# Kernel optimization log

Measured on AMD Instinct MI355X. Metric: run time of the kernel, lower is better.

## Reference

```python
import jax, jax.numpy as jnp
import numpy as np

C_IN, C_OUT, H = 8, 8, 16
N1D = 20                      # 1D quadrature points -> 400 mesh nodes in 2D
B = 16
DECAY = (N1D / 4.0) ** 4      # set_quad: decay_param = (N/4)**4


def _quad_mesh():
    # Gauss-Legendre nodes/weights on [-1,1], tensor-product in 2D (get_quad_mesh)
    x, w = np.polynomial.legendre.leggauss(N1D)
    X, Y = np.meshgrid(x, x, indexing='xy')
    WX, WY = np.meshgrid(w, w, indexing='xy')
    nodes = np.dstack([X, Y]).reshape(-1, 2).astype(np.float32)
    weights = (WX * WY).reshape(-1).astype(np.float32)
    return nodes, weights


def setup_inputs() -> dict:
    key = jax.random.key(0)
    k1, k2, k3, k4 = jax.random.split(key, 4)
    nodes, w = _quad_mesh()
    K = C_IN * C_OUT
    return {
        'features': jax.random.normal(k1, (B, C_IN, N1D * N1D), jnp.float32),
        # 64 tiny MLPs (Linear no bias + Sin), spec (2,16,16,1), stacked on axis 0
        'W1': jax.random.normal(k2, (K, H, 2), jnp.float32) / np.sqrt(2.0),
        'W2': jax.random.normal(k3, (K, H, H), jnp.float32) / np.sqrt(float(H)),
        'W3': jax.random.normal(k4, (K, 1, H), jnp.float32) / np.sqrt(float(H)),
        'output_locs': jnp.asarray(nodes),   # (M,2) same tensor-product mesh
        'mesh_nodes': jnp.asarray(nodes),    # (N,2)
        'mesh_weights': jnp.asarray(w),      # (N,) product of 1D weights
    }


def _kernel(W1, W2, W3, output_locs, mesh_nodes):
    # pairwise eval points z = y_m - x_n, shape (M, N, 2)
    z = output_locs[:, None, :] - mesh_nodes[None, :, :]
    M, N, _ = z.shape
    zf = z.reshape(M * N, 2)
    # batched tiny MLPs: Linear -> Sin -> Linear -> Sin -> Linear (no bias)
    h = jnp.sin(jnp.einsum('khd,pd->kph', W1, zf))
    h = jnp.sin(jnp.einsum('koh,kph->kpo', W2, h))
    kv = jnp.einsum('koh,kph->kpo', W3, h)[..., 0]          # (K, M*N)
    # bump function enforcing compact support: exp(1 - 1/(1 - c*||z||^4))
    bump_arg = jnp.sum(zf * zf, axis=-1) ** 2               # ||z||^4
    inside = bump_arg < 1.0 / DECAY
    safe = jnp.where(inside, 1.0 - DECAY * bump_arg, 1.0)
    bump = jnp.where(inside, jnp.exp(1.0 - 1.0 / safe), 0.0)
    kv = kv * bump[None, :]
    return kv.reshape(C_OUT, C_IN, M, N)


def reference(features, W1, W2, W3, output_locs, mesh_nodes, mesh_weights):
    Kmat = _kernel(W1, W2, W3, output_locs, mesh_nodes)     # (Co,Ci,M,N)
    # quadrature-weighted conv sum: out[b,o,m] = sum_{i,n} K[o,i,m,n] w[n] f[b,i,n]
    return jnp.einsum('oimn,n,bin->bom', Kmat, mesh_weights, features)
```

## Files before the change

### kernel.cpp

```cpp
#include <hip/hip_runtime.h>
#include <math.h>

#define CIN   8
#define COUT  8
#define HH    16
#define NN    400
#define MM    400
#define BB    16

#define THREADS 512
#define PMAX    32
#define NGRP    16
#define MPG     25
#define PPG     16
#define NPAGES  (NGRP*PPG)
#define MAXNM   12

#define WS_FT   0
#define WS_L    (NN*CIN*BB)
#define WS_CNT  (WS_L + MM*PMAX*4)
#define WS_PM0  (WS_CNT + MM)
#define WS_PNM  (WS_PM0 + NPAGES)

__device__ __forceinline__ bool bump_inside(float zx, float zy, float& a) {
    float s = __fadd_rn(__fmul_rn(zx, zx), __fmul_rn(zy, zy));
    a = __fmul_rn(s, s);
    return a < (1.0f / 625.0f);
}

__global__ __launch_bounds__(THREADS) void prep_kernel(
    const float* __restrict__ f,
    const float* __restrict__ locs,
    const float* __restrict__ nodes,
    const float* __restrict__ wq,
    float* __restrict__ ws)
{
    const int blk = blockIdx.x;
    const int t   = threadIdx.x;

    if (blk < 100) {
        int idx = blk * 512 + t;
        int b = idx / 3200;
        int r = idx - b * 3200;
        int i = r / 400;
        int n = r - i * 400;
        ws[WS_FT + n*128 + i*16 + b] = f[idx];
    } else if (blk < 150) {
        const int lane = t & 63;
        const int w    = t >> 6;
        const int m    = (blk - 100) * 8 + w;
        const float2 y = ((const float2*)locs)[m];
        const float2* nd = (const float2*)nodes;
        float4* lst = (float4*)(ws + WS_L);
        int cnt = 0;
        for (int n0 = 0; n0 < NN; n0 += 64) {
            int n = n0 + lane;
            bool in = false;
            float zx = 0.f, zy = 0.f, bwv = 0.f;
            if (n < NN) {
                float2 x = nd[n];
                zx = y.x - x.x; zy = y.y - x.y;
                float a;
                if (bump_inside(zx, zy, a)) {
                    in = true;
                    bwv = __expf(1.0f - 1.0f/(1.0f - 625.0f*a)) * wq[n];
                }
            }
            unsigned long long msk = __ballot(in);
            int idx = cnt + __popcll(msk & ((1ull << lane) - 1ull));
            if (in && idx < PMAX)
                lst[m*PMAX + idx] = make_float4(zx, zy, bwv, __int_as_float(n));
            cnt += __popcll(msk);
        }
        if (lane >= cnt && lane < PMAX)
            lst[m*PMAX + lane] = make_float4(0.f, 0.f, 0.f, __int_as_float(0));
    } else {
        __shared__ float dx2[400], dy2[400];
        __shared__ int   scnt[400];
        if (t < 400) {
            int i = t / 20, j = t % 20;
            float zx = locs[2*i]          - nodes[2*j];
            float zy = locs[2*(i*20) + 1] - nodes[2*(j*20) + 1];
            dx2[t] = __fmul_rn(zx, zx);
            dy2[t] = __fmul_rn(zy, zy);
        }
        __syncthreads();
        if (t < 400) {
            int mx = t % 20, my = t / 20;
            int c = 0;
            for (int ny = 0; ny < 20; ++ny) {
                float dyv = dy2[my*20 + ny];
                for (int nx = 0; nx < 20; ++nx) {
                    float s = __fadd_rn(dx2[mx*20 + nx], dyv);
                    float a = __fmul_rn(s, s);
                    c += (a < (1.0f / 625.0f)) ? 1 : 0;
                }
            }
            c = min(c, PMAX);
            scnt[t] = c;
            ((int*)ws)[WS_CNT + t] = c;
        }
        __syncthreads();
        if (t < NGRP) {
            int* pm0 = (int*)ws + WS_PM0;
            int* pnm = (int*)ws + WS_PNM;
            const int m0g = t * MPG, mend = m0g + MPG;
            int p = t * PPG;
            int cur0 = m0g, used = 0;
            for (int m = m0g; m < mend; ++m) {
                int c = scnt[m];
                if (used + c > 64) {
                    pm0[p] = cur0; pnm[p] = m - cur0; ++p;
                    cur0 = m; used = 0;
                }
                used += c;
            }
            pm0[p] = cur0; pnm[p] = mend - cur0; ++p;
            for (; p < (t + 1) * PPG; ++p) { pm0[p] = 0; pnm[p] = 0; }
        }
    }
}

__global__ __launch_bounds__(THREADS) void quadconv_kernel(
    const float* __restrict__ W1,
    const float* __restrict__ W2,
    const float* __restrict__ W3,
    const float* __restrict__ ws,
    float* __restrict__ out)
{
    __shared__ float s_w2[8*256];
    __shared__ float s_w1[8*32];
    __shared__ float s_w3[8*16];
    __shared__ float s_kv[8*64];
    __shared__ int   s_pn[64];
    __shared__ int   s_off[MAXNM + 1];
    __shared__ int   s_m0;

    const int t    = threadIdx.x;
    const int lane = t & 63;
    const int w    = __builtin_amdgcn_readfirstlane(t >> 6);
    const int p    = blockIdx.x >> 3;
    const int kg   = blockIdx.x & 7;

    const int nm = ((const int*)ws)[WS_PNM + p];
    if (nm == 0) return;

    {
        const float4* W2v = (const float4*)(W2 + kg * 8 * 256);
        ((float4*)s_w2)[t] = W2v[t];
        if (t < 64) ((float4*)s_w1)[t] = ((const float4*)(W1 + kg * 8 * 32))[t];
        if (t < 32) ((float4*)s_w3)[t] = ((const float4*)(W3 + kg * 8 * 16))[t];
    }
    if (t == 0) {
        int m0 = ((const int*)ws)[WS_PM0 + p];
        s_m0 = m0;
        int off = 0;
        s_off[0] = 0;
        for (int j = 0; j < nm; ++j) {
            off += ((const int*)ws)[WS_CNT + m0 + j];
            s_off[j + 1] = off;
        }
    }
    __syncthreads();

    int seg = 0;
    #pragma unroll
    for (int sgi = 1; sgi < MAXNM; ++sgi)
        seg += (sgi < nm && lane >= s_off[sgi]) ? 1 : 0;
    const int used = s_off[nm];
    float4 sv = make_float4(0.f, 0.f, 0.f, 0.f);
    int n_id = 0;
    if (lane < used) {
        const int m  = s_m0 + seg;
        const int jj = lane - s_off[seg];
        sv = ((const float4*)(ws + WS_L))[m * PMAX + jj];
        n_id = __float_as_int(sv.w);
    }
    if (t < 64) s_pn[t] = n_id;

    {
        const float* __restrict__ w1 = s_w1 + w * 32;
        const float* __restrict__ w2 = s_w2 + w * 256;
        const float* __restrict__ w3 = s_w3 + w * 16;
        const float zx = sv.x, zy = sv.y, bw = sv.z;

        float h1[HH];
        #pragma unroll
        for (int j = 0; j < HH; ++j)
            h1[j] = __sinf(w1[2*j] * zx + w1[2*j + 1] * zy);

        float kv = 0.f;
        #pragma unroll
        for (int oo = 0; oo < HH; ++oo) {
            float d = 0.f;
            #pragma unroll
            for (int j = 0; j < HH; ++j)
                d += w2[oo*HH + j] * h1[j];
            kv += w3[oo] * __sinf(d);
        }
        s_kv[w*64 + lane] = kv * bw;
    }
    __syncthreads();

    if (t < nm * 16) {
        const int b    = t & 15;
        const int sidx = t >> 4;
        const int lo   = s_off[sidx];
        const int L    = s_off[sidx + 1] - lo;
        const float* __restrict__ ftp = ws + WS_FT;
        float acc = 0.f;
        for (int j = 0; j < L; ++j) {
            const int n = s_pn[lo + j];
            const float* fb = ftp + n*128 + b;
            #pragma unroll
            for (int ww = 0; ww < 8; ++ww)
                acc += s_kv[ww*64 + lo + j] * fb[ww*16];
        }
        out[b * (COUT*MM) + kg * MM + (s_m0 + sidx)] = acc;
    }
}

extern "C" void kernel_launch(void* const* d_in, const int* in_sizes, int n_in,
                              void* d_out, int out_size, void* d_ws, size_t ws_size,
                              hipStream_t stream) {
    const float* f     = (const float*)d_in[0];
    const float* W1    = (const float*)d_in[1];
    const float* W2    = (const float*)d_in[2];
    const float* W3    = (const float*)d_in[3];
    const float* locs  = (const float*)d_in[4];
    const float* nodes = (const float*)d_in[5];
    const float* wq    = (const float*)d_in[6];
    float* out = (float*)d_out;
    float* ws  = (float*)d_ws;

    prep_kernel<<<dim3(151), dim3(THREADS), 0, stream>>>(f, locs, nodes, wq, ws);
    quadconv_kernel<<<dim3(NPAGES * 8), dim3(THREADS), 0, stream>>>(
        W1, W2, W3, ws, out);
}
```

Baseline: 26.80 us.

## Transpose feature layout and split reduction into parallel partial products

Reorders the transposed feature workspace to [n][b][ci] so each thread can fetch 8 input channels with two float4 loads. All 512 threads now compute per-point partial sums over input channels into a padded shared buffer, and the final per-output reduction only sums those partials. The serial offset prefix in thread 0 becomes a wave shuffle scan. This adds one extra barrier and shared buffer, in exchange for removing the serial, scattered-gather inner loop.

```diff
diff --git a/kernel.cpp b/kernel.cpp
--- a/kernel.cpp
+++ b/kernel.cpp
@@ -44,7 +44,7 @@
         int r = idx - b * 3200;
         int i = r / 400;
         int n = r - i * 400;
-        ws[WS_FT + n*128 + i*16 + b] = f[idx];
+        ws[WS_FT + n*128 + b*8 + i] = f[idx];
     } else if (blk < 150) {
         const int lane = t & 63;
         const int w    = t >> 6;
@@ -132,6 +132,7 @@
     __shared__ float s_w1[8*32];
     __shared__ float s_w3[8*16];
     __shared__ float s_kv[8*64];
+    __shared__ float s_pp[64*17];
     __shared__ int   s_pn[64];
     __shared__ int   s_off[MAXNM + 1];
     __shared__ int   s_m0;
@@ -144,6 +145,7 @@
 
     const int nm = ((const int*)ws)[WS_PNM + p];
     if (nm == 0) return;
+    const int m0 = ((const int*)ws)[WS_PM0 + p];
 
     {
         const float4* W2v = (const float4*)(W2 + kg * 8 * 256);
@@ -151,15 +153,15 @@
         if (t < 64) ((float4*)s_w1)[t] = ((const float4*)(W1 + kg * 8 * 32))[t];
         if (t < 32) ((float4*)s_w3)[t] = ((const float4*)(W3 + kg * 8 * 16))[t];
     }
-    if (t == 0) {
-        int m0 = ((const int*)ws)[WS_PM0 + p];
-        s_m0 = m0;
-        int off = 0;
-        s_off[0] = 0;
-        for (int j = 0; j < nm; ++j) {
-            off += ((const int*)ws)[WS_CNT + m0 + j];
-            s_off[j + 1] = off;
-        }
+    if (w == 0) {
+        int c = (lane < nm) ? ((const int*)ws)[WS_CNT + m0 + lane] : 0;
+        #pragma unroll
+        for (int d = 1; d < 16; d <<= 1) {
+            int u = __shfl_up(c, d);
+            if (lane >= d) c += u;
+        }
+        if (lane < nm) s_off[lane + 1] = c;
+        if (lane == 0) { s_off[0] = 0; s_m0 = m0; }
     }
     __syncthreads();
 
@@ -171,7 +173,7 @@
     float4 sv = make_float4(0.f, 0.f, 0.f, 0.f);
     int n_id = 0;
     if (lane < used) {
-        const int m  = s_m0 + seg;
+        const int m  = m0 + seg;
         const int jj = lane - s_off[seg];
         sv = ((const float4*)(ws + WS_L))[m * PMAX + jj];
         n_id = __float_as_int(sv.w);
@@ -202,20 +204,36 @@
     }
     __syncthreads();
 
+    {
+        const int j  = t >> 3;
+        const int b0 = t & 7;
+        const int n  = s_pn[j];
+        const float* __restrict__ fb = ws + WS_FT + n*128;
+        float4 A0 = *(const float4*)(fb + b0*8);
+        float4 A1 = *(const float4*)(fb + b0*8 + 4);
+        float4 B0 = *(const float4*)(fb + (b0+8)*8);
+        float4 B1 = *(const float4*)(fb + (b0+8)*8 + 4);
+        float k0 = s_kv[0*64 + j], k1 = s_kv[1*64 + j];
+        float k2 = s_kv[2*64 + j], k3 = s_kv[3*64 + j];
+        float k4 = s_kv[4*64 + j], k5 = s_kv[5*64 + j];
+        float k6 = s_kv[6*64 + j], k7 = s_kv[7*64 + j];
+        float pA = k0*A0.x + k1*A0.y + k2*A0.z + k3*A0.w
+                 + k4*A1.x + k5*A1.y + k6*A1.z + k7*A1.w;
+        float pB = k0*B0.x + k1*B0.y + k2*B0.z + k3*B0.w
+                 + k4*B1.x + k5*B1.y + k6*B1.z + k7*B1.w;
+        s_pp[j*17 + b0]     = pA;
+        s_pp[j*17 + b0 + 8] = pB;
+    }
+    __syncthreads();
+
     if (t < nm * 16) {
         const int b    = t & 15;
         const int sidx = t >> 4;
         const int lo   = s_off[sidx];
-        const int L    = s_off[sidx + 1] - lo;
-        const float* __restrict__ ftp = ws + WS_FT;
+        const int hi   = s_off[sidx + 1];
         float acc = 0.f;
-        for (int j = 0; j < L; ++j) {
-            const int n = s_pn[lo + j];
-            const float* fb = ftp + n*128 + b;
-            #pragma unroll
-            for (int ww = 0; ww < 8; ++ww)
-                acc += s_kv[ww*64 + lo + j] * fb[ww*16];
-        }
+        for (int j = lo; j < hi; ++j)
+            acc += s_pp[j*17 + b];
         out[b * (COUT*MM) + kg * MM + (s_m0 + sidx)] = acc;
     }
 }
```

Result: faster. 24.24 us (-9.5%).
